# Kernel optimization log

Measured on AMD Instinct MI355X. Metric: run time of the kernel, lower is better.

The kernel has to match this reference:

```python
import math
import jax, jax.numpy as jnp
import numpy as np

B, S, H, M, E = 4, 4096, 1024, 1024, 16
CAPACITY_FACTOR = 2.0
ROUTE_SCALE = 1.0


def setup_inputs() -> dict:
    key = jax.random.key(0)
    ks = jax.random.split(key, 8)
    return {
        "hidden_states": jax.random.normal(ks[0], (B, S, H), dtype=jnp.float32),
        "hidden_states_unmodulated": jax.random.normal(ks[1], (B, S, H), dtype=jnp.float32),
        "timestep": jax.random.normal(ks[2], (B, H), dtype=jnp.float32),
        "gate_w": jax.random.normal(ks[3], (2 * H, E), dtype=jnp.float32) * 0.02,
        "gate_up_proj": jax.random.normal(ks[4], (E, H, 2 * M), dtype=jnp.float32) * 0.02,
        "down_proj": jax.random.normal(ks[5], (E, M, H), dtype=jnp.float32) * 0.02,
        "shared_gate_up_w": jax.random.normal(ks[6], (H, 2 * M), dtype=jnp.float32) * 0.02,
        "shared_down_w": jax.random.normal(ks[7], (M, H), dtype=jnp.float32) * 0.02,
    }


def reference(hidden_states, hidden_states_unmodulated, timestep, gate_w,
              gate_up_proj, down_proj, shared_gate_up_w, shared_down_w):
    b, s, h = hidden_states.shape
    e = gate_up_proj.shape[0]
    capacity = max(1, math.ceil(CAPACITY_FACTOR * s / e))  # static per shapes

    # --- router ---
    t = jnp.broadcast_to(timestep[:, None, :], (b, s, h))
    router_input = jnp.concatenate([t, hidden_states_unmodulated], axis=-1)  # [b,s,2h]
    logits = router_input @ gate_w                                           # [b,s,e]
    scores = jax.nn.sigmoid(logits.astype(jnp.float32)).astype(logits.dtype)
    affinity = jnp.swapaxes(scores, 1, 2)                                    # [b,e,s]

    # --- expert-choice top-k ---
    gating, top_idx = jax.lax.top_k(affinity, capacity)                      # [b,e,cap]
    offsets = (jnp.arange(b) * s)[:, None, None]
    gidx = jnp.swapaxes(offsets + top_idx, 0, 1).reshape(-1)                 # [e*b*cap]
    gflat = jnp.swapaxes(gating, 0, 1).reshape(-1)

    # normalize per-token scores over experts that picked the token
    sums = jnp.zeros(b * s, dtype=gflat.dtype).at[gidx].add(gflat)
    gflat = gflat / (sums[gidx] + 1e-12) * ROUTE_SCALE

    # --- dispatch + grouped SwiGLU experts ---
    x_flat = hidden_states.reshape(b * s, h)
    routed = x_flat[gidx].reshape(e, b * capacity, h)
    gu = jnp.einsum('eth,ehf->etf', routed, gate_up_proj)                    # [e,t,2m]
    g, u = jnp.split(gu, 2, axis=-1)
    expert_out = jnp.einsum('etm,emh->eth', jax.nn.silu(g) * u, down_proj)
    expert_out = expert_out.reshape(e * b * capacity, h)
    expert_out = (expert_out.astype(jnp.float32) *
                  gflat.astype(jnp.float32)[:, None]).astype(hidden_states.dtype)

    # --- shared expert (SwiGLUProj order: hidden * silu(gate)) ---
    hgu = hidden_states @ shared_gate_up_w                                   # [b,s,2m]
    hs_, hg = jnp.split(hgu, 2, axis=-1)
    shared = (hs_ * jax.nn.silu(hg)) @ shared_down_w                         # [b,s,h]

    # --- scatter combine ---
    out = shared.reshape(b * s, h).at[gidx].add(expert_out)
    return out.reshape(b, s, h)
```

## Files before the change

kernel.cpp:

```cpp
#include <hip/hip_runtime.h>
#include <math.h>

#define Bb 4
#define Ss 4096
#define Hh 1024
#define Mm 1024
#define Ee 16
#define CAPk 512

typedef unsigned short u16;
typedef __attribute__((ext_vector_type(8))) short short8;
typedef __attribute__((ext_vector_type(4))) float floatx4;
typedef __attribute__((ext_vector_type(4))) unsigned short ushort4v;

__device__ __forceinline__ float silu_f(float x) {
    return x / (1.0f + expf(-x));
}

__device__ __forceinline__ u16 f2b(float x) {
    union { float f; unsigned u; } v; v.f = x;
    unsigned r = (v.u + 0x7fffu + ((v.u >> 16) & 1u)) >> 16;
    return (u16)r;
}

__device__ __forceinline__ void gl_lds16(const void* g, void* l) {
    __builtin_amdgcn_global_load_lds((const __attribute__((address_space(1))) void*)g,
                                     (__attribute__((address_space(3))) void*)l, 16, 0, 0);
}


__global__ __launch_bounds__(64)
void tlogit_kernel(const float* __restrict__ timestep,
                   const float* __restrict__ gate_w,
                   float* __restrict__ tlogit) {
    int be = blockIdx.x;
    int b = be >> 4, e = be & 15;
    int lane = threadIdx.x;
    float p = 0.f;
#pragma unroll
    for (int j = 0; j < 16; ++j) {
        int h = lane + 64 * j;
        p += timestep[b * Hh + h] * gate_w[h * Ee + e];
    }
#pragma unroll
    for (int off = 32; off; off >>= 1) p += __shfl_xor(p, off);
    if (lane == 0) tlogit[be] = p;
}

__global__ __launch_bounds__(256)
void router_scores(const float* __restrict__ hsu,
                   const float* __restrict__ gate_w,
                   const float* __restrict__ tlogit,
                   float* __restrict__ scores) {
    __shared__ float Xs[64 * 64];
    __shared__ float Gs[64 * 16];
    const int t = threadIdx.x;
    const int row0 = blockIdx.x * 64;
    const int b = row0 >> 12;
    const int wave = t >> 6, lane = t & 63;
    const int e0 = wave * 4;
    const float* gw2 = gate_w + (size_t)Hh * Ee;

    float acc0 = 0.f, acc1 = 0.f, acc2 = 0.f, acc3 = 0.f;

    for (int k0 = 0; k0 < Hh; k0 += 64) {
        __syncthreads();
#pragma unroll
        for (int r = 0; r < 4; ++r) {
            int tok = r * 16 + (t >> 4);
            int cslot = t & 15;
            int g = cslot ^ (tok & 15);
            const float* src = hsu + (size_t)(row0 + tok) * Hh + k0 + g * 4;
            char* dst = (char*)Xs + r * 4096 + wave * 1024;
            gl_lds16(src, dst);
        }
        {
            const float* src = gw2 + (size_t)k0 * Ee + t * 4;
            char* dst = (char*)Gs + wave * 1024;
            gl_lds16(src, dst);
        }
        __syncthreads();
#pragma unroll
        for (int kk = 0; kk < 64; kk += 4) {
            int slot = (kk >> 2) ^ (lane & 15);
            float4 a = *(const float4*)&Xs[lane * 64 + slot * 4];
            float4 g0 = *(const float4*)&Gs[(kk + 0) * Ee + e0];
            float4 g1 = *(const float4*)&Gs[(kk + 1) * Ee + e0];
            float4 g2 = *(const float4*)&Gs[(kk + 2) * Ee + e0];
            float4 g3 = *(const float4*)&Gs[(kk + 3) * Ee + e0];
            acc0 += a.x * g0.x; acc0 += a.y * g1.x; acc0 += a.z * g2.x; acc0 += a.w * g3.x;
            acc1 += a.x * g0.y; acc1 += a.y * g1.y; acc1 += a.z * g2.y; acc1 += a.w * g3.y;
            acc2 += a.x * g0.z; acc2 += a.y * g1.z; acc2 += a.z * g2.z; acc2 += a.w * g3.z;
            acc3 += a.x * g0.w; acc3 += a.y * g1.w; acc3 += a.z * g2.w; acc3 += a.w * g3.w;
        }
    }
    const int s = (row0 + lane) & (Ss - 1);
    float l0 = acc0 + tlogit[b * Ee + e0 + 0];
    float l1 = acc1 + tlogit[b * Ee + e0 + 1];
    float l2 = acc2 + tlogit[b * Ee + e0 + 2];
    float l3 = acc3 + tlogit[b * Ee + e0 + 3];
    scores[((size_t)(b * Ee + e0 + 0)) * Ss + s] = 1.f / (1.f + expf(-l0));
    scores[((size_t)(b * Ee + e0 + 1)) * Ss + s] = 1.f / (1.f + expf(-l1));
    scores[((size_t)(b * Ee + e0 + 2)) * Ss + s] = 1.f / (1.f + expf(-l2));
    scores[((size_t)(b * Ee + e0 + 3)) * Ss + s] = 1.f / (1.f + expf(-l3));
}

__global__ __launch_bounds__(256)
void topk_kernel(const float* __restrict__ scores,
                 int* __restrict__ sel_idx,
                 float* __restrict__ sel_gate) {
    const int be = blockIdx.x;
    const float* sc = scores + (size_t)be * Ss;
    const int t = threadIdx.x;
    __shared__ unsigned hist[256];
    __shared__ unsigned sh_prefix;
    __shared__ int sh_need;
    __shared__ unsigned eqoff[256];
    __shared__ unsigned cnt_gt;

    unsigned vu[16];
#pragma unroll
    for (int i = 0; i < 16; ++i) vu[i] = __float_as_uint(sc[t * 16 + i]);

    unsigned prefix = 0;
    int need = CAPk;
    for (int pass = 0; pass < 4; ++pass) {
        const int shift = 24 - 8 * pass;
        hist[t] = 0;
        __syncthreads();
#pragma unroll
        for (int i = 0; i < 16; ++i) {
            unsigned u = vu[i];
            bool ok = (pass == 0) || ((u >> (shift + 8)) == prefix);
            if (ok) atomicAdd(&hist[(u >> shift) & 255u], 1u);
        }
        __syncthreads();
        if (t == 0) {
            int nd = need;
            int bin = 255;
            for (; bin >= 0; --bin) {
                int c = (int)hist[bin];
                if (c < nd) nd -= c; else break;
            }
            sh_prefix = (prefix << 8) | (unsigned)bin;
            sh_need = nd;
        }
        __syncthreads();
        prefix = sh_prefix;
        need = sh_need;
        __syncthreads();
    }
    const unsigned T = prefix;
    const int need_eq = need;
    const unsigned ngt = (unsigned)(CAPk - need_eq);

    int myeq = 0;
#pragma unroll
    for (int i = 0; i < 16; ++i) myeq += (vu[i] == T) ? 1 : 0;
    eqoff[t] = (unsigned)myeq;
    if (t == 0) cnt_gt = 0;
    __syncthreads();
    if (t == 0) {
        unsigned run = 0;
        for (int j = 0; j < 256; ++j) { unsigned c = eqoff[j]; eqoff[j] = run; run += c; }
    }
    __syncthreads();
    unsigned eqr = eqoff[t];
#pragma unroll
    for (int i = 0; i < 16; ++i) {
        unsigned u = vu[i];
        int s = t * 16 + i;
        if (u > T) {
            unsigned slot = atomicAdd(&cnt_gt, 1u);
            sel_idx[(size_t)be * CAPk + slot] = s;
            sel_gate[(size_t)be * CAPk + slot] = __uint_as_float(u);
        } else if (u == T) {
            if ((int)eqr < need_eq) {
                unsigned slot = ngt + eqr;
                sel_idx[(size_t)be * CAPk + slot] = s;
                sel_gate[(size_t)be * CAPk + slot] = __uint_as_float(u);
            }
            eqr++;
        }
    }
}

__global__ void zero_kernel(float* p, int n) {
    int i = blockIdx.x * 256 + threadIdx.x;
    if (i < n) p[i] = 0.f;
}

__global__ void accum_kernel(const int* __restrict__ sel_idx,
                             const float* __restrict__ sel_gate,
                             float* __restrict__ sums) {
    int g = blockIdx.x * 256 + threadIdx.x;
    int be = g / CAPk;
    int b = be >> 4;
    atomicAdd(&sums[b * Ss + sel_idx[g]], sel_gate[g]);
}

__global__ void finalize_kernel(const int* __restrict__ sel_idx,
                                const float* __restrict__ sel_gate,
                                const float* __restrict__ sums,
                                int* __restrict__ slot_token,
                                float* __restrict__ slot_w) {
    int g = blockIdx.x * 256 + threadIdx.x;
    int be = g / CAPk, c = g % CAPk;
    int b = be >> 4, e = be & 15;
    int token = b * Ss + sel_idx[g];
    float wv = sel_gate[g] / (sums[token] + 1e-12f);
    int o = (e * Bb + b) * CAPk + c;
    slot_token[o] = token;
    slot_w[o] = wv;
}


__global__ __launch_bounds__(256)
void convert_bf16(const float* __restrict__ src, u16* __restrict__ dst) {
    int i = (blockIdx.x * 256 + threadIdx.x) * 4;
    float4 v = *(const float4*)(src + i);
    ushort4v o = { f2b(v.x), f2b(v.y), f2b(v.z), f2b(v.w) };
    *(ushort4v*)(dst + i) = o;
}

__global__ __launch_bounds__(256)
void transpose_bf16(const float* __restrict__ W, u16* __restrict__ Wt,
                    int N, size_t zsrc, size_t zdst) {
    __shared__ float tile[32][33];
    int n0 = blockIdx.x * 32, k0 = blockIdx.y * 32, z = blockIdx.z;
    const float* Ws = W + (size_t)z * zsrc;
    u16* Wd = Wt + (size_t)z * zdst;
    int tn = threadIdx.x & 31, tk = threadIdx.x >> 5;
#pragma unroll
    for (int i = 0; i < 4; ++i)
        tile[tk + i * 8][tn] = Ws[(size_t)(k0 + tk + i * 8) * N + n0 + tn];
    __syncthreads();
#pragma unroll
    for (int i = 0; i < 4; ++i)
        Wd[(size_t)(n0 + tk + i * 8) * 1024 + k0 + tn] = f2b(tile[tn][tk + i * 8]);
}

__global__ __launch_bounds__(256)
void gather_bf16(const float* __restrict__ X, const int* __restrict__ slot_token,
                 u16* __restrict__ Ag, int e0) {
    int z = blockIdx.x >> 11, li = blockIdx.x & 2047;
    int token = slot_token[(e0 + z) * 2048 + li];
    const float* src = X + (size_t)token * 1024;
    u16* dst = Ag + (size_t)blockIdx.x * 1024;
    int i = threadIdx.x * 4;
    float4 v = *(const float4*)(src + i);
    ushort4v o = { f2b(v.x), f2b(v.y), f2b(v.z), f2b(v.w) };
    *(ushort4v*)(dst + i) = o;
}


__device__ __forceinline__ void stage_tile(const u16* __restrict__ grow, int k0,
                                           u16* lds, int t) {
#pragma unroll
    for (int r = 0; r < 4; ++r) {
        int o = (r * 256 + t) * 16;
        int m = o >> 7;
        int c = ((o >> 4) & 7) ^ (m & 7);
        const u16* src = grow + (size_t)m * 1024 + k0 + c * 8;
        u16* dst = lds + ((r * 4096 + (t >> 6) * 1024) >> 1);
        gl_lds16(src, dst);
    }
}

template <bool SILU_FIRST>
__global__ __launch_bounds__(256, 2)
void gemm1_mfma(const u16* __restrict__ A, int a_row0, int zstride,
                const u16* __restrict__ W1t, u16* __restrict__ act) {
    __shared__ u16 lA[128 * 64];
    __shared__ u16 lB1[128 * 64];
    __shared__ u16 lB2[128 * 64];
    const int t = threadIdx.x;
    const int n0 = blockIdx.x * 128;
    const int bm0 = blockIdx.y * 128;
    const int z = blockIdx.z;
    const int zb = z * zstride;
    const u16* Arow = A + (size_t)(a_row0 + zb + bm0) * 1024;
    const u16* B1row = W1t + ((size_t)z * 2048 + n0) * 1024;
    const u16* B2row = B1row + (size_t)1024 * 1024;
    const int lane = t & 63;
    const int wv = t >> 6, wm = wv & 1, wn = wv >> 1;
    const int quad = lane >> 4, l15 = lane & 15;

    floatx4 zero4 = {0.f, 0.f, 0.f, 0.f};
    floatx4 acc1[4][4], acc2[4][4];
#pragma unroll
    for (int i = 0; i < 4; ++i)
#pragma unroll
        for (int j = 0; j < 4; ++j) { acc1[i][j] = zero4; acc2[i][j] = zero4; }

    for (int k0 = 0; k0 < 1024; k0 += 64) {
        __syncthreads();
        stage_tile(Arow, k0, lA, t);
        stage_tile(B1row, k0, lB1, t);
        stage_tile(B2row, k0, lB2, t);
        __syncthreads();
#pragma unroll
        for (int kc = 0; kc < 2; ++kc) {
            short8 af[4], bf1[4], bf2[4];
#pragma unroll
            for (int mi = 0; mi < 4; ++mi) {
                int m = wm * 64 + mi * 16 + l15;
                int off = m * 64 + (((kc * 4 + quad) ^ (m & 7)) * 8);
                af[mi] = *(const short8*)&lA[off];
            }
#pragma unroll
            for (int ni = 0; ni < 4; ++ni) {
                int n = wn * 64 + ni * 16 + l15;
                int off = n * 64 + (((kc * 4 + quad) ^ (n & 7)) * 8);
                bf1[ni] = *(const short8*)&lB1[off];
                bf2[ni] = *(const short8*)&lB2[off];
            }
#pragma unroll
            for (int mi = 0; mi < 4; ++mi)
#pragma unroll
                for (int ni = 0; ni < 4; ++ni) {
                    acc1[mi][ni] = __builtin_amdgcn_mfma_f32_16x16x32_bf16(af[mi], bf1[ni], acc1[mi][ni], 0, 0, 0);
                    acc2[mi][ni] = __builtin_amdgcn_mfma_f32_16x16x32_bf16(af[mi], bf2[ni], acc2[mi][ni], 0, 0, 0);
                }
        }
    }
#pragma unroll
    for (int mi = 0; mi < 4; ++mi)
#pragma unroll
        for (int ni = 0; ni < 4; ++ni)
#pragma unroll
            for (int r = 0; r < 4; ++r) {
                int m = wm * 64 + mi * 16 + quad * 4 + r;
                int n = wn * 64 + ni * 16 + l15;
                float c1 = acc1[mi][ni][r], c2 = acc2[mi][ni][r];
                float v = SILU_FIRST ? silu_f(c1) * c2 : c1 * silu_f(c2);
                act[(size_t)(zb + bm0 + m) * 1024 + n0 + n] = f2b(v);
            }
}

template <bool SCATTER>
__global__ __launch_bounds__(256, 2)
void gemm2_mfma(const u16* __restrict__ A, int zstride,
                const u16* __restrict__ W2t,
                const int* __restrict__ slot_token, const float* __restrict__ slot_w,
                float* __restrict__ out, int out_row0, int e_base) {
    __shared__ u16 lA[128 * 64];
    __shared__ u16 lB[128 * 64];
    __shared__ int s_tok[128];
    __shared__ float s_w[128];
    const int t = threadIdx.x;
    const int n0 = blockIdx.x * 128;
    const int bm0 = blockIdx.y * 128;
    const int z = blockIdx.z;
    const int zb = z * zstride;
    const u16* Arow = A + (size_t)(zb + bm0) * 1024;
    const u16* Brow = W2t + ((size_t)z * 1024 + n0) * 1024;
    const int lane = t & 63;
    const int wv = t >> 6, wm = wv & 1, wn = wv >> 1;
    const int quad = lane >> 4, l15 = lane & 15;

    if (SCATTER && t < 128) {
        int gi = (e_base + z) * 2048 + bm0 + t;
        s_tok[t] = slot_token[gi];
        s_w[t] = slot_w[gi];
    }

    floatx4 zero4 = {0.f, 0.f, 0.f, 0.f};
    floatx4 acc[4][4];
#pragma unroll
    for (int i = 0; i < 4; ++i)
#pragma unroll
        for (int j = 0; j < 4; ++j) acc[i][j] = zero4;

    for (int k0 = 0; k0 < 1024; k0 += 64) {
        __syncthreads();
        stage_tile(Arow, k0, lA, t);
        stage_tile(Brow, k0, lB, t);
        __syncthreads();
#pragma unroll
        for (int kc = 0; kc < 2; ++kc) {
            short8 af[4], bf[4];
#pragma unroll
            for (int mi = 0; mi < 4; ++mi) {
                int m = wm * 64 + mi * 16 + l15;
                int off = m * 64 + (((kc * 4 + quad) ^ (m & 7)) * 8);
                af[mi] = *(const short8*)&lA[off];
            }
#pragma unroll
            for (int ni = 0; ni < 4; ++ni) {
                int n = wn * 64 + ni * 16 + l15;
                int off = n * 64 + (((kc * 4 + quad) ^ (n & 7)) * 8);
                bf[ni] = *(const short8*)&lB[off];
            }
#pragma unroll
            for (int mi = 0; mi < 4; ++mi)
#pragma unroll
                for (int ni = 0; ni < 4; ++ni)
                    acc[mi][ni] = __builtin_amdgcn_mfma_f32_16x16x32_bf16(af[mi], bf[ni], acc[mi][ni], 0, 0, 0);
        }
    }
#pragma unroll
    for (int mi = 0; mi < 4; ++mi)
#pragma unroll
        for (int ni = 0; ni < 4; ++ni)
#pragma unroll
            for (int r = 0; r < 4; ++r) {
                int m = wm * 64 + mi * 16 + quad * 4 + r;
                int n = wn * 64 + ni * 16 + l15;
                float c = acc[mi][ni][r];
                if (SCATTER) {
                    atomicAdd(&out[(size_t)s_tok[m] * 1024 + n0 + n], c * s_w[m]);
                } else {
                    out[(size_t)(out_row0 + bm0 + m) * 1024 + n0 + n] = c;
                }
            }
}


extern "C" void kernel_launch(void* const* d_in, const int* in_sizes, int n_in,
                              void* d_out, int out_size, void* d_ws, size_t ws_size,
                              hipStream_t stream) {
    const float* hidden   = (const float*)d_in[0];
    const float* hsu      = (const float*)d_in[1];
    const float* timestep = (const float*)d_in[2];
    const float* gate_w   = (const float*)d_in[3];
    const float* gate_up  = (const float*)d_in[4];
    const float* down     = (const float*)d_in[5];
    const float* sh_gu    = (const float*)d_in[6];
    const float* sh_dn    = (const float*)d_in[7];
    float* out = (float*)d_out;

    char* p = (char*)d_ws;
    auto alloc = [&](size_t bytes) { char* r = p; p += (bytes + 255) & ~(size_t)255; return r; };
    float* tlogit    = (float*)alloc((size_t)Bb * Ee * 4);
    float* scores    = (float*)alloc((size_t)Bb * Ee * Ss * 4);
    int*   sel_idx   = (int*)  alloc((size_t)Bb * Ee * CAPk * 4);
    float* sel_gate  = (float*)alloc((size_t)Bb * Ee * CAPk * 4);
    float* sums      = (float*)alloc((size_t)Bb * Ss * 4);
    int*   slot_token= (int*)  alloc((size_t)Ee * Bb * CAPk * 4);
    float* slot_w    = (float*)alloc((size_t)Ee * Bb * CAPk * 4);
    char* phase = p;
    long long avail = (long long)((char*)d_ws + ws_size - phase);
    if (avail < 0) avail = 0;

    tlogit_kernel<<<Bb * Ee, 64, 0, stream>>>(timestep, gate_w, tlogit);
    router_scores<<<(Bb * Ss) / 64, 256, 0, stream>>>(hsu, gate_w, tlogit, scores);
    topk_kernel<<<Bb * Ee, 256, 0, stream>>>(scores, sel_idx, sel_gate);
    zero_kernel<<<(Bb * Ss + 255) / 256, 256, 0, stream>>>(sums, Bb * Ss);
    accum_kernel<<<(Bb * Ee * CAPk) / 256, 256, 0, stream>>>(sel_idx, sel_gate, sums);
    finalize_kernel<<<(Bb * Ee * CAPk) / 256, 256, 0, stream>>>(sel_idx, sel_gate, sums,
                                                                slot_token, slot_w);

    {
        u16* Xb   = (u16*)phase;
        u16* Wt1s = Xb + (size_t)16384 * 1024;
        u16* Wt2s = Wt1s + (size_t)2048 * 1024;
        u16* actS = Wt2s + (size_t)1024 * 1024;
        long long fixed = ((long long)16384 * 1024 + 2048 * 1024 + 1024 * 1024) * 2;
        long long room = (avail - fixed) / 2048;
        room &= ~127LL;
        int R = (int)(room > 16384 ? 16384 : room);
        if (R < 128) R = 128;

        convert_bf16<<<16384, 256, 0, stream>>>(hidden, Xb);
        transpose_bf16<<<dim3(64, 32, 1), 256, 0, stream>>>(sh_gu, Wt1s, 2048, 0, 0);
        transpose_bf16<<<dim3(32, 32, 1), 256, 0, stream>>>(sh_dn, Wt2s, 1024, 0, 0);
        for (int r0 = 0; r0 < Bb * Ss; r0 += R) {
            int cur = Bb * Ss - r0; if (cur > R) cur = R;
            gemm1_mfma<false><<<dim3(8, cur / 128, 1), 256, 0, stream>>>(Xb, r0, 0, Wt1s, actS);
            gemm2_mfma<false><<<dim3(8, cur / 128, 1), 256, 0, stream>>>(actS, 0, Wt2s,
                                                                         nullptr, nullptr, out, r0, 0);
        }
    }

    {
        const long long per_e = ((long long)2048 * 1024 * 3 + 1024 * 1024) * 2;
        int g = (int)(avail / per_e);
        if (g < 1) g = 1;
        if (g > Ee) g = Ee;
        u16* Ag   = (u16*)phase;
        u16* Wt1r = Ag   + (size_t)g * 2048 * 1024;
        u16* Wt2r = Wt1r + (size_t)g * 2048 * 1024;
        u16* actR = Wt2r + (size_t)g * 1024 * 1024;

        for (int e0 = 0; e0 < Ee; e0 += g) {
            int cg = Ee - e0; if (cg > g) cg = g;
            gather_bf16<<<cg * 2048, 256, 0, stream>>>(hidden, slot_token, Ag, e0);
            transpose_bf16<<<dim3(64, 32, cg), 256, 0, stream>>>(
                gate_up + (size_t)e0 * 2097152, Wt1r, 2048, 2097152, 2097152);
            transpose_bf16<<<dim3(32, 32, cg), 256, 0, stream>>>(
                down + (size_t)e0 * 1048576, Wt2r, 1024, 1048576, 1048576);
            gemm1_mfma<true><<<dim3(8, 16, cg), 256, 0, stream>>>(Ag, 0, 2048, Wt1r, actR);
            gemm2_mfma<true><<<dim3(8, 16, cg), 256, 0, stream>>>(actR, 2048, Wt2r,
                                                                  slot_token, slot_w, out, 0, e0);
        }
    }
}
```

Measured before the change: 881.7 us.

## Replace atomic scatter with inverse-index gather fused into shared-expert GEMM epilogue

```diff
diff --git a/kernel.cpp b/kernel.cpp
--- a/kernel.cpp
+++ b/kernel.cpp
@@ -29,28 +29,10 @@
 }
 
 
-__global__ __launch_bounds__(64)
-void tlogit_kernel(const float* __restrict__ timestep,
-                   const float* __restrict__ gate_w,
-                   float* __restrict__ tlogit) {
-    int be = blockIdx.x;
-    int b = be >> 4, e = be & 15;
-    int lane = threadIdx.x;
-    float p = 0.f;
-#pragma unroll
-    for (int j = 0; j < 16; ++j) {
-        int h = lane + 64 * j;
-        p += timestep[b * Hh + h] * gate_w[h * Ee + e];
-    }
-#pragma unroll
-    for (int off = 32; off; off >>= 1) p += __shfl_xor(p, off);
-    if (lane == 0) tlogit[be] = p;
-}
-
 __global__ __launch_bounds__(256)
 void router_scores(const float* __restrict__ hsu,
                    const float* __restrict__ gate_w,
-                   const float* __restrict__ tlogit,
+                   const float* __restrict__ timestep,
                    float* __restrict__ scores) {
     __shared__ float Xs[64 * 64];
     __shared__ float Gs[64 * 16];
@@ -60,6 +42,23 @@
     const int wave = t >> 6, lane = t & 63;
     const int e0 = wave * 4;
     const float* gw2 = gate_w + (size_t)Hh * Ee;
+
+    float tl0 = 0.f, tl1 = 0.f, tl2 = 0.f, tl3 = 0.f;
+    {
+        const float* tsrow = timestep + (size_t)b * Hh;
+#pragma unroll
+        for (int j = 0; j < 16; ++j) {
+            int h = lane + 64 * j;
+            float tv = tsrow[h];
+            const float* gw = gate_w + (size_t)h * Ee + e0;
+            tl0 += tv * gw[0]; tl1 += tv * gw[1]; tl2 += tv * gw[2]; tl3 += tv * gw[3];
+        }
+#pragma unroll
+        for (int off = 32; off; off >>= 1) {
+            tl0 += __shfl_xor(tl0, off); tl1 += __shfl_xor(tl1, off);
+            tl2 += __shfl_xor(tl2, off); tl3 += __shfl_xor(tl3, off);
+        }
+    }
 
     float acc0 = 0.f, acc1 = 0.f, acc2 = 0.f, acc3 = 0.f;
 
@@ -95,10 +94,10 @@
         }
     }
     const int s = (row0 + lane) & (Ss - 1);
-    float l0 = acc0 + tlogit[b * Ee + e0 + 0];
-    float l1 = acc1 + tlogit[b * Ee + e0 + 1];
-    float l2 = acc2 + tlogit[b * Ee + e0 + 2];
-    float l3 = acc3 + tlogit[b * Ee + e0 + 3];
+    float l0 = acc0 + tl0;
+    float l1 = acc1 + tl1;
+    float l2 = acc2 + tl2;
+    float l3 = acc3 + tl3;
     scores[((size_t)(b * Ee + e0 + 0)) * Ss + s] = 1.f / (1.f + expf(-l0));
     scores[((size_t)(b * Ee + e0 + 1)) * Ss + s] = 1.f / (1.f + expf(-l1));
     scores[((size_t)(b * Ee + e0 + 2)) * Ss + s] = 1.f / (1.f + expf(-l2));
@@ -112,10 +111,11 @@
     const int be = blockIdx.x;
     const float* sc = scores + (size_t)be * Ss;
     const int t = threadIdx.x;
+    const int lane = t & 63, w = t >> 6;
     __shared__ unsigned hist[256];
+    __shared__ unsigned wtot[4];
     __shared__ unsigned sh_prefix;
     __shared__ int sh_need;
-    __shared__ unsigned eqoff[256];
     __shared__ unsigned cnt_gt;
 
     unsigned vu[16];
@@ -135,15 +135,22 @@
             if (ok) atomicAdd(&hist[(u >> shift) & 255u], 1u);
         }
         __syncthreads();
-        if (t == 0) {
-            int nd = need;
-            int bin = 255;
-            for (; bin >= 0; --bin) {
-                int c = (int)hist[bin];
-                if (c < nd) nd -= c; else break;
-            }
-            sh_prefix = (prefix << 8) | (unsigned)bin;
-            sh_need = nd;
+        unsigned hval = hist[t];
+        unsigned s = hval;
+#pragma unroll
+        for (int d = 1; d < 64; d <<= 1) {
+            unsigned o = __shfl_down(s, d);
+            if (lane + d < 64) s += o;
+        }
+        if (lane == 0) wtot[w] = s;
+        __syncthreads();
+#pragma unroll
+        for (int w2 = 0; w2 < 4; ++w2)
+            if (w2 > w) s += wtot[w2];
+        unsigned Snext = s - hval;
+        if (s >= (unsigned)need && Snext < (unsigned)need) {
+            sh_prefix = (prefix << 8) | (unsigned)t;
+            sh_need = need - (int)Snext;
         }
         __syncthreads();
         prefix = sh_prefix;
@@ -157,15 +164,19 @@
     int myeq = 0;
 #pragma unroll
     for (int i = 0; i < 16; ++i) myeq += (vu[i] == T) ? 1 : 0;
-    eqoff[t] = (unsigned)myeq;
+    unsigned e = (unsigned)myeq;
+#pragma unroll
+    for (int d = 1; d < 64; d <<= 1) {
+        unsigned o = __shfl_up(e, d);
+        if (lane >= d) e += o;
+    }
+    if (lane == 63) wtot[w] = e;
     if (t == 0) cnt_gt = 0;
     __syncthreads();
-    if (t == 0) {
-        unsigned run = 0;
-        for (int j = 0; j < 256; ++j) { unsigned c = eqoff[j]; eqoff[j] = run; run += c; }
-    }
-    __syncthreads();
-    unsigned eqr = eqoff[t];
+    unsigned eqr = e - (unsigned)myeq;
+#pragma unroll
+    for (int w2 = 0; w2 < 4; ++w2)
+        if (w2 < w) eqr += wtot[w2];
 #pragma unroll
     for (int i = 0; i < 16; ++i) {
         unsigned u = vu[i];
@@ -185,9 +196,10 @@
     }
 }
 
-__global__ void zero_kernel(float* p, int n) {
+__global__ void zero2_kernel(float* __restrict__ sums, int* __restrict__ cnt) {
     int i = blockIdx.x * 256 + threadIdx.x;
-    if (i < n) p[i] = 0.f;
+    sums[i] = 0.f;
+    cnt[i] = 0;
 }
 
 __global__ void accum_kernel(const int* __restrict__ sel_idx,
@@ -203,7 +215,9 @@
                                 const float* __restrict__ sel_gate,
                                 const float* __restrict__ sums,
                                 int* __restrict__ slot_token,
-                                float* __restrict__ slot_w) {
+                                float* __restrict__ slot_w,
+                                int* __restrict__ cnt,
+                                int* __restrict__ inv) {
     int g = blockIdx.x * 256 + threadIdx.x;
     int be = g / CAPk, c = g % CAPk;
     int b = be >> 4, e = be & 15;
@@ -212,6 +226,8 @@
     int o = (e * Bb + b) * CAPk + c;
     slot_token[o] = token;
     slot_w[o] = wv;
+    int pos = atomicAdd(&cnt[token], 1);
+    inv[(size_t)token * 16 + pos] = o;
 }
 
 
@@ -226,18 +242,29 @@
 __global__ __launch_bounds__(256)
 void transpose_bf16(const float* __restrict__ W, u16* __restrict__ Wt,
                     int N, size_t zsrc, size_t zdst) {
-    __shared__ float tile[32][33];
-    int n0 = blockIdx.x * 32, k0 = blockIdx.y * 32, z = blockIdx.z;
+    __shared__ float tile[64][65];
+    int n0 = blockIdx.x * 64, k0 = blockIdx.y * 64, z = blockIdx.z;
     const float* Ws = W + (size_t)z * zsrc;
     u16* Wd = Wt + (size_t)z * zdst;
-    int tn = threadIdx.x & 31, tk = threadIdx.x >> 5;
-#pragma unroll
-    for (int i = 0; i < 4; ++i)
-        tile[tk + i * 8][tn] = Ws[(size_t)(k0 + tk + i * 8) * N + n0 + tn];
+    int t = threadIdx.x;
+    int lr = t >> 4, lc = (t & 15) * 4;
+#pragma unroll
+    for (int i = 0; i < 4; ++i) {
+        float4 v = *(const float4*)&Ws[(size_t)(k0 + lr + i * 16) * N + n0 + lc];
+        tile[lr + i * 16][lc + 0] = v.x;
+        tile[lr + i * 16][lc + 1] = v.y;
+        tile[lr + i * 16][lc + 2] = v.z;
+        tile[lr + i * 16][lc + 3] = v.w;
+    }
     __syncthreads();
-#pragma unroll
-    for (int i = 0; i < 4; ++i)
-        Wd[(size_t)(n0 + tk + i * 8) * 1024 + k0 + tn] = f2b(tile[tn][tk + i * 8]);
+    int on = t >> 2;
+    int ok0 = (t & 3) * 16;
+    u16 buf[16];
+#pragma unroll
+    for (int j = 0; j < 16; ++j) buf[j] = f2b(tile[ok0 + j][on]);
+    u16* dp = &Wd[(size_t)(n0 + on) * 1024 + k0 + ok0];
+    *(short8*)(dp) = *(short8*)&buf[0];
+    *(short8*)(dp + 8) = *(short8*)&buf[8];
 }
 
 __global__ __launch_bounds__(256)
@@ -338,16 +365,20 @@
             }
 }
 
-template <bool SCATTER>
+template <int MODE>
 __global__ __launch_bounds__(256, 2)
 void gemm2_mfma(const u16* __restrict__ A, int zstride,
                 const u16* __restrict__ W2t,
                 const int* __restrict__ slot_token, const float* __restrict__ slot_w,
-                float* __restrict__ out, int out_row0, int e_base) {
+                float* __restrict__ out, int out_row0, int e_base,
+                const int* __restrict__ cnt, const int* __restrict__ inv,
+                const float* __restrict__ eo) {
     __shared__ u16 lA[128 * 64];
     __shared__ u16 lB[128 * 64];
-    __shared__ int s_tok[128];
-    __shared__ float s_w[128];
+    __shared__ int s_tok[(MODE == 1) ? 128 : 1];
+    __shared__ float s_w[(MODE == 1 || MODE == 2) ? 128 : 1];
+    __shared__ int s_cnt[(MODE == 3) ? 128 : 1];
+    __shared__ int s_inv[(MODE == 3) ? 128 * 16 : 1];
     const int t = threadIdx.x;
     const int n0 = blockIdx.x * 128;
     const int bm0 = blockIdx.y * 128;
@@ -359,10 +390,15 @@
     const int wv = t >> 6, wm = wv & 1, wn = wv >> 1;
     const int quad = lane >> 4, l15 = lane & 15;
 
-    if (SCATTER && t < 128) {
+    if ((MODE == 1 || MODE == 2) && t < 128) {
         int gi = (e_base + z) * 2048 + bm0 + t;
-        s_tok[t] = slot_token[gi];
+        if (MODE == 1) s_tok[t] = slot_token[gi];
         s_w[t] = slot_w[gi];
+    }
+    if (MODE == 3) {
+        int base = out_row0 + bm0;
+        if (t < 128) s_cnt[t] = cnt[base + t];
+        for (int j = t; j < 128 * 16; j += 256) s_inv[j] = inv[(size_t)base * 16 + j];
     }
 
     floatx4 zero4 = {0.f, 0.f, 0.f, 0.f};
@@ -408,8 +444,16 @@
                 int m = wm * 64 + mi * 16 + quad * 4 + r;
                 int n = wn * 64 + ni * 16 + l15;
                 float c = acc[mi][ni][r];
-                if (SCATTER) {
+                if (MODE == 1) {
                     atomicAdd(&out[(size_t)s_tok[m] * 1024 + n0 + n], c * s_w[m]);
+                } else if (MODE == 2) {
+                    out[((size_t)((e_base + z) * 2048 + bm0 + m)) * 1024 + n0 + n] = c * s_w[m];
+                } else if (MODE == 3) {
+                    float v = c;
+                    int kc2 = s_cnt[m];
+                    for (int j = 0; j < kc2; ++j)
+                        v += eo[(size_t)s_inv[m * 16 + j] * 1024 + n0 + n];
+                    out[(size_t)(out_row0 + bm0 + m) * 1024 + n0 + n] = v;
                 } else {
                     out[(size_t)(out_row0 + bm0 + m) * 1024 + n0 + n] = c;
                 }
@@ -432,67 +476,124 @@
 
     char* p = (char*)d_ws;
     auto alloc = [&](size_t bytes) { char* r = p; p += (bytes + 255) & ~(size_t)255; return r; };
-    float* tlogit    = (float*)alloc((size_t)Bb * Ee * 4);
     float* scores    = (float*)alloc((size_t)Bb * Ee * Ss * 4);
     int*   sel_idx   = (int*)  alloc((size_t)Bb * Ee * CAPk * 4);
     float* sel_gate  = (float*)alloc((size_t)Bb * Ee * CAPk * 4);
     float* sums      = (float*)alloc((size_t)Bb * Ss * 4);
     int*   slot_token= (int*)  alloc((size_t)Ee * Bb * CAPk * 4);
     float* slot_w    = (float*)alloc((size_t)Ee * Bb * CAPk * 4);
+    int*   cnt       = (int*)  alloc((size_t)Bb * Ss * 4);
+    int*   inv       = (int*)  alloc((size_t)Bb * Ss * 16 * 4);
     char* phase = p;
     long long avail = (long long)((char*)d_ws + ws_size - phase);
     if (avail < 0) avail = 0;
 
-    tlogit_kernel<<<Bb * Ee, 64, 0, stream>>>(timestep, gate_w, tlogit);
-    router_scores<<<(Bb * Ss) / 64, 256, 0, stream>>>(hsu, gate_w, tlogit, scores);
+    const long long eo_bytes     = (long long)32768 * 1024 * 4;
+    const long long shared_fixed = ((long long)16384 * 1024 + 2048 * 1024 + 1024 * 1024) * 2;
+    const long long per_e        = ((long long)2048 * 1024 * 3 + 1024 * 1024) * 2;
+
+    router_scores<<<(Bb * Ss) / 64, 256, 0, stream>>>(hsu, gate_w, timestep, scores);
     topk_kernel<<<Bb * Ee, 256, 0, stream>>>(scores, sel_idx, sel_gate);
-    zero_kernel<<<(Bb * Ss + 255) / 256, 256, 0, stream>>>(sums, Bb * Ss);
+    zero2_kernel<<<(Bb * Ss) / 256, 256, 0, stream>>>(sums, cnt);
     accum_kernel<<<(Bb * Ee * CAPk) / 256, 256, 0, stream>>>(sel_idx, sel_gate, sums);
     finalize_kernel<<<(Bb * Ee * CAPk) / 256, 256, 0, stream>>>(sel_idx, sel_gate, sums,
-                                                                slot_token, slot_w);
-
-    {
-        u16* Xb   = (u16*)phase;
-        u16* Wt1s = Xb + (size_t)16384 * 1024;
-        u16* Wt2s = Wt1s + (size_t)2048 * 1024;
-        u16* actS = Wt2s + (size_t)1024 * 1024;
-        long long fixed = ((long long)16384 * 1024 + 2048 * 1024 + 1024 * 1024) * 2;
-        long long room = (avail - fixed) / 2048;
-        room &= ~127LL;
-        int R = (int)(room > 16384 ? 16384 : room);
-        if (R < 128) R = 128;
-
-        convert_bf16<<<16384, 256, 0, stream>>>(hidden, Xb);
-        transpose_bf16<<<dim3(64, 32, 1), 256, 0, stream>>>(sh_gu, Wt1s, 2048, 0, 0);
-        transpose_bf16<<<dim3(32, 32, 1), 256, 0, stream>>>(sh_dn, Wt2s, 1024, 0, 0);
-        for (int r0 = 0; r0 < Bb * Ss; r0 += R) {
-            int cur = Bb * Ss - r0; if (cur > R) cur = R;
-            gemm1_mfma<false><<<dim3(8, cur / 128, 1), 256, 0, stream>>>(Xb, r0, 0, Wt1s, actS);
-            gemm2_mfma<false><<<dim3(8, cur / 128, 1), 256, 0, stream>>>(actS, 0, Wt2s,
-                                                                         nullptr, nullptr, out, r0, 0);
-        }
-    }
-
-    {
-        const long long per_e = ((long long)2048 * 1024 * 3 + 1024 * 1024) * 2;
-        int g = (int)(avail / per_e);
-        if (g < 1) g = 1;
-        if (g > Ee) g = Ee;
-        u16* Ag   = (u16*)phase;
-        u16* Wt1r = Ag   + (size_t)g * 2048 * 1024;
-        u16* Wt2r = Wt1r + (size_t)g * 2048 * 1024;
-        u16* actR = Wt2r + (size_t)g * 1024 * 1024;
-
-        for (int e0 = 0; e0 < Ee; e0 += g) {
-            int cg = Ee - e0; if (cg > g) cg = g;
-            gather_bf16<<<cg * 2048, 256, 0, stream>>>(hidden, slot_token, Ag, e0);
-            transpose_bf16<<<dim3(64, 32, cg), 256, 0, stream>>>(
-                gate_up + (size_t)e0 * 2097152, Wt1r, 2048, 2097152, 2097152);
-            transpose_bf16<<<dim3(32, 32, cg), 256, 0, stream>>>(
-                down + (size_t)e0 * 1048576, Wt2r, 1024, 1048576, 1048576);
-            gemm1_mfma<true><<<dim3(8, 16, cg), 256, 0, stream>>>(Ag, 0, 2048, Wt1r, actR);
-            gemm2_mfma<true><<<dim3(8, 16, cg), 256, 0, stream>>>(actR, 2048, Wt2r,
-                                                                  slot_token, slot_w, out, 0, e0);
-        }
-    }
-}
+                                                                slot_token, slot_w, cnt, inv);
+
+    bool use_eo = (avail >= eo_bytes + shared_fixed + (long long)128 * 2048) &&
+                  (avail - eo_bytes >= per_e);
+
+    if (use_eo) {
+        float* eo = (float*)phase;
+        char* ph2 = phase + eo_bytes;
+        long long avail2 = avail - eo_bytes;
+
+        {
+            int g = (int)(avail2 / per_e);
+            if (g < 1) g = 1;
+            if (g > Ee) g = Ee;
+            u16* Ag   = (u16*)ph2;
+            u16* Wt1r = Ag   + (size_t)g * 2048 * 1024;
+            u16* Wt2r = Wt1r + (size_t)g * 2048 * 1024;
+            u16* actR = Wt2r + (size_t)g * 1024 * 1024;
+
+            for (int e0 = 0; e0 < Ee; e0 += g) {
+                int cg = Ee - e0; if (cg > g) cg = g;
+                gather_bf16<<<cg * 2048, 256, 0, stream>>>(hidden, slot_token, Ag, e0);
+                transpose_bf16<<<dim3(32, 16, cg), 256, 0, stream>>>(
+                    gate_up + (size_t)e0 * 2097152, Wt1r, 2048, 2097152, 2097152);
+                transpose_bf16<<<dim3(16, 16, cg), 256, 0, stream>>>(
+                    down + (size_t)e0 * 1048576, Wt2r, 1024, 1048576, 1048576);
+                gemm1_mfma<true><<<dim3(8, 16, cg), 256, 0, stream>>>(Ag, 0, 2048, Wt1r, actR);
+                gemm2_mfma<2><<<dim3(8, 16, cg), 256, 0, stream>>>(actR, 2048, Wt2r,
+                                                                   slot_token, slot_w, eo, 0, e0,
+                                                                   nullptr, nullptr, nullptr);
+            }
+        }
+
+        {
+            u16* Xb   = (u16*)ph2;
+            u16* Wt1s = Xb + (size_t)16384 * 1024;
+            u16* Wt2s = Wt1s + (size_t)2048 * 1024;
+            u16* actS = Wt2s + (size_t)1024 * 1024;
+            long long room = (avail2 - shared_fixed) / 2048;
+            room &= ~127LL;
+            int R = (int)(room > 16384 ? 16384 : room);
+            if (R < 128) R = 128;
+
+            convert_bf16<<<16384, 256, 0, stream>>>(hidden, Xb);
+            transpose_bf16<<<dim3(32, 16, 1), 256, 0, stream>>>(sh_gu, Wt1s, 2048, 0, 0);
+            transpose_bf16<<<dim3(16, 16, 1), 256, 0, stream>>>(sh_dn, Wt2s, 1024, 0, 0);
+            for (int r0 = 0; r0 < Bb * Ss; r0 += R) {
+                int cur = Bb * Ss - r0; if (cur > R) cur = R;
+                gemm1_mfma<false><<<dim3(8, cur / 128, 1), 256, 0, stream>>>(Xb, r0, 0, Wt1s, actS);
+                gemm2_mfma<3><<<dim3(8, cur / 128, 1), 256, 0, stream>>>(actS, 0, Wt2s,
+                                                                         nullptr, nullptr, out, r0, 0,
+                                                                         cnt, inv, eo);
+            }
+        }
+    } else {
+        {
+            u16* Xb   = (u16*)phase;
+            u16* Wt1s = Xb + (size_t)16384 * 1024;
+            u16* Wt2s = Wt1s + (size_t)2048 * 1024;
+            u16* actS = Wt2s + (size_t)1024 * 1024;
+            long long room = (avail - shared_fixed) / 2048;
+            room &= ~127LL;
+            int R = (int)(room > 16384 ? 16384 : room);
+            if (R < 128) R = 128;
+
+            convert_bf16<<<16384, 256, 0, stream>>>(hidden, Xb);
+            transpose_bf16<<<dim3(32, 16, 1), 256, 0, stream>>>(sh_gu, Wt1s, 2048, 0, 0);
+            transpose_bf16<<<dim3(16, 16, 1), 256, 0, stream>>>(sh_dn, Wt2s, 1024, 0, 0);
+            for (int r0 = 0; r0 < Bb * Ss; r0 += R) {
+                int cur = Bb * Ss - r0; if (cur > R) cur = R;
+                gemm1_mfma<false><<<dim3(8, cur / 128, 1), 256, 0, stream>>>(Xb, r0, 0, Wt1s, actS);
+                gemm2_mfma<0><<<dim3(8, cur / 128, 1), 256, 0, stream>>>(actS, 0, Wt2s,
+                                                                         nullptr, nullptr, out, r0, 0,
+                                                                         nullptr, nullptr, nullptr);
+            }
+        }
+        {
+            int g = (int)(avail / per_e);
+            if (g < 1) g = 1;
+            if (g > Ee) g = Ee;
+            u16* Ag   = (u16*)phase;
+            u16* Wt1r = Ag   + (size_t)g * 2048 * 1024;
+            u16* Wt2r = Wt1r + (size_t)g * 2048 * 1024;
+            u16* actR = Wt2r + (size_t)g * 1024 * 1024;
+
+            for (int e0 = 0; e0 < Ee; e0 += g) {
+                int cg = Ee - e0; if (cg > g) cg = g;
+                gather_bf16<<<cg * 2048, 256, 0, stream>>>(hidden, slot_token, Ag, e0);
+                transpose_bf16<<<dim3(32, 16, cg), 256, 0, stream>>>(
+                    gate_up + (size_t)e0 * 2097152, Wt1r, 2048, 2097152, 2097152);
+                transpose_bf16<<<dim3(16, 16, cg), 256, 0, stream>>>(
+                    down + (size_t)e0 * 1048576, Wt2r, 1024, 1048576, 1048576);
+                gemm1_mfma<true><<<dim3(8, 16, cg), 256, 0, stream>>>(Ag, 0, 2048, Wt1r, actR);
+                gemm2_mfma<1><<<dim3(8, 16, cg), 256, 0, stream>>>(actR, 2048, Wt2r,
+                                                                   slot_token, slot_w, out, 0, e0,
+                                                                   nullptr, nullptr, nullptr);
+            }
+        }
+    }
+}
```

Result: slower. 1.016 ms (+15.3%).
